# Kernel tuning notes

Hardware: AMD Instinct MI355X
Metric: run time of the kernel (lower is better)

## Reference

```python
import jax, jax.numpy as jnp
import numpy as np


def setup_inputs() -> dict:
    key = jax.random.key(0)
    k1, k2, k3 = jax.random.split(key, 3)
    B, D, C = 16384, 1024, 14
    z_image = jax.random.normal(k1, (B, D), dtype=jnp.float32)
    z_text = jax.random.normal(k2, (B, D), dtype=jnp.float32)
    labels = jax.random.randint(k3, (B, C), 0, 2, dtype=jnp.int32)
    return {"z_image": z_image, "z_text": z_text, "labels": labels}


def _margins(labels):
    # labels: [B, C] binary; imposter index j = (i+1) % B -> roll by -1
    lj = jnp.roll(labels, -1, axis=0)
    equal = jnp.all(labels == lj, axis=1)                     # [B]
    n = jnp.sum(labels | lj, axis=1).astype(jnp.float32)      # union size
    d = jnp.sum(labels ^ lj, axis=1).astype(jnp.float32)      # hamming diff
    m = jnp.where(n > 0, jnp.maximum(0.5, d / jnp.maximum(n, 1.0)), 0.5)
    return jnp.where(equal, 0.0, m)                           # [B]


def reference(z_image, z_text, labels):
    # similarity_function == 'dot' (default path of the torch module)
    margin = _margins(labels)                                  # [B]
    paired = jnp.sum(z_image * z_text, axis=1)                 # dot(img_i, txt_i)
    imp_img = jnp.sum(jnp.roll(z_image, -1, axis=0) * z_text, axis=1)  # dot(img_j, txt_i)
    imp_txt = jnp.sum(jnp.roll(z_text, -1, axis=0) * z_image, axis=1)  # dot(txt_j, img_i)
    loss_img = jnp.mean(jax.nn.relu(imp_img - paired + margin))
    loss_txt = jnp.mean(jax.nn.relu(imp_txt - paired + margin))
    return loss_img + loss_txt
```

## Files before the change

kernel.cpp:

```cpp
#include <hip/hip_runtime.h>


constexpr int D      = 1024;
constexpr int C      = 14;
constexpr int TPR    = 16;
constexpr int RPB    = 256 / TPR;
constexpr int CHUNKS = D / 4 / TPR;

__device__ __forceinline__ float dot4(const float4 x, const float4 y) {
    return x.x * y.x + x.y * y.y + x.z * y.z + x.w * y.w;
}

__global__ __launch_bounds__(256, 2) void rank_phase1(
    const float* __restrict__ zi, const float* __restrict__ zt,
    const int* __restrict__ labels, float* __restrict__ partial, int B)
{
    const int t    = threadIdx.x;
    const int rsub = t >> 4;
    const int csub = t & 15;
    const int row  = blockIdx.x * RPB + rsub;
    const int M    = B - 1;
    const int nrow = (row + 1) & M;

    float margin = 0.f;
    if (csub == 0) {
        const int2* La = (const int2*)(labels + (size_t)row  * C);
        const int2* Lb = (const int2*)(labels + (size_t)nrow * C);
        int dv = 0, nv = 0;
        #pragma unroll
        for (int q = 0; q < C / 2; ++q) {
            const int2 x = La[q];
            const int2 y = Lb[q];
            dv += (x.x ^ y.x) + (x.y ^ y.y);
            nv += (x.x | y.x) + (x.y | y.y);
        }
        margin = (dv == 0) ? 0.f : fmaxf(0.5f, (float)dv / (float)nv);
    }

    const float4* Ar  = (const float4*)(zi + (size_t)row  * D);
    const float4* Br  = (const float4*)(zt + (size_t)row  * D);
    const float4* Ar1 = (const float4*)(zi + (size_t)nrow * D);
    const float4* Br1 = (const float4*)(zt + (size_t)nrow * D);

    float p = 0.f, ii = 0.f, it = 0.f;
    #pragma unroll
    for (int c = 0; c < CHUNKS; ++c) {
        const int idx = csub + TPR * c;
        const float4 a  = Ar [idx];
        const float4 b  = Br [idx];
        const float4 a1 = Ar1[idx];
        const float4 b1 = Br1[idx];
        p  += dot4(a,  b);
        ii += dot4(a1, b);
        it += dot4(b1, a);
    }

    #pragma unroll
    for (int off = 1; off < TPR; off <<= 1) {
        p  += __shfl_xor(p,  off, 64);
        ii += __shfl_xor(ii, off, 64);
        it += __shfl_xor(it, off, 64);
    }

    __shared__ float sm[RPB];
    if (csub == 0)
        sm[rsub] = fmaxf(ii - p + margin, 0.f)
                 + fmaxf(it - p + margin, 0.f);
    __syncthreads();
    if (t == 0) {
        float s = 0.f;
        #pragma unroll
        for (int k = 0; k < RPB; ++k) s += sm[k];
        partial[blockIdx.x] = s;
    }
}

__global__ __launch_bounds__(256) void rank_phase2(
    const float* __restrict__ partial, float* __restrict__ out,
    int npart, float invB)
{
    float s = 0.f;
    for (int i = threadIdx.x; i < npart; i += 256) s += partial[i];
    #pragma unroll
    for (int off = 32; off > 0; off >>= 1) s += __shfl_down(s, off, 64);
    __shared__ float sm[4];
    if ((threadIdx.x & 63) == 0) sm[threadIdx.x >> 6] = s;
    __syncthreads();
    if (threadIdx.x == 0)
        out[0] = (sm[0] + sm[1] + sm[2] + sm[3]) * invB;
}

extern "C" void kernel_launch(void* const* d_in, const int* in_sizes, int n_in,
                              void* d_out, int out_size, void* d_ws, size_t ws_size,
                              hipStream_t stream) {
    const float* zi     = (const float*)d_in[0];
    const float* zt     = (const float*)d_in[1];
    const int*   labels = (const int*)d_in[2];
    float*       out    = (float*)d_out;
    float*       ws     = (float*)d_ws;

    const int B      = in_sizes[0] / D;
    const int blocks = B / RPB;

    rank_phase1<<<blocks, 256, 0, stream>>>(zi, zt, labels, ws, B);
    rank_phase2<<<1, 256, 0, stream>>>(ws, out, blocks, 1.0f / (float)B);
}
```

Measured before the change: 155.7 us.

## Share neighbor rows via wave shuffles and split columns across waves

Each wave now processes eight consecutive rows over a quarter of the columns and obtains the next row's vectors through lane shuffles instead of reloading them from memory, with only a single halo row loaded extra. Loads use nontemporal hints to avoid polluting cache. Margin computation and the per-row hinge are moved to a final per-block step after combining wave partials in shared memory. This reduces redundant global reads but adds shuffle work and a divergent halo load.

```diff
diff --git a/kernel.cpp b/kernel.cpp
--- a/kernel.cpp
+++ b/kernel.cpp
@@ -1,31 +1,96 @@
 #include <hip/hip_runtime.h>
 
 
-constexpr int D      = 1024;
-constexpr int C      = 14;
-constexpr int TPR    = 16;
-constexpr int RPB    = 256 / TPR;
-constexpr int CHUNKS = D / 4 / TPR;
+constexpr int D   = 1024;
+constexpr int C   = 14;
+constexpr int RPB = 8;
+constexpr int CPR = D / 4;
 
-__device__ __forceinline__ float dot4(const float4 x, const float4 y) {
+typedef float f4 __attribute__((ext_vector_type(4)));
+
+__device__ __forceinline__ float dot4(const f4 x, const f4 y) {
     return x.x * y.x + x.y * y.y + x.z * y.z + x.w * y.w;
 }
 
-__global__ __launch_bounds__(256, 2) void rank_phase1(
+__device__ __forceinline__ f4 shfl_down4(const f4 v) {
+    f4 r;
+    r.x = __shfl_down(v.x, 8, 64);
+    r.y = __shfl_down(v.y, 8, 64);
+    r.z = __shfl_down(v.z, 8, 64);
+    r.w = __shfl_down(v.w, 8, 64);
+    return r;
+}
+
+__global__ __launch_bounds__(256) void rank_phase1(
     const float* __restrict__ zi, const float* __restrict__ zt,
     const int* __restrict__ labels, float* __restrict__ partial, int B)
 {
-    const int t    = threadIdx.x;
-    const int rsub = t >> 4;
-    const int csub = t & 15;
-    const int row  = blockIdx.x * RPB + rsub;
+    const int wave = threadIdx.x >> 6;
+    const int lane = threadIdx.x & 63;
+    const int r0   = blockIdx.x * RPB;
     const int M    = B - 1;
-    const int nrow = (row + 1) & M;
 
-    float margin = 0.f;
-    if (csub == 0) {
-        const int2* La = (const int2*)(labels + (size_t)row  * C);
-        const int2* Lb = (const int2*)(labels + (size_t)nrow * C);
+    const int row_off = lane >> 3;
+    const int cl      = lane & 7;
+    const int row     = r0 + row_off;
+    const int hrow    = (r0 + RPB) & M;
+
+    const f4* ZI = (const f4*)zi;
+    const f4* ZT = (const f4*)zt;
+
+    const int cb = wave * (CPR / 4);
+
+    float p = 0.f, ii = 0.f, it = 0.f;
+
+    #pragma unroll
+    for (int i = 0; i < CPR / 4 / 8; ++i) {
+        const int c = cb + 8 * i + cl;
+        const f4 a = __builtin_nontemporal_load(&ZI[(size_t)row * CPR + c]);
+        const f4 b = __builtin_nontemporal_load(&ZT[(size_t)row * CPR + c]);
+
+        f4 ha, hb;
+        if (row_off == 7) {
+            ha = __builtin_nontemporal_load(&ZI[(size_t)hrow * CPR + c]);
+            hb = __builtin_nontemporal_load(&ZT[(size_t)hrow * CPR + c]);
+        }
+
+        f4 aN = shfl_down4(a);
+        f4 bN = shfl_down4(b);
+        if (row_off == 7) { aN = ha; bN = hb; }
+
+        p  += dot4(a,  b);
+        ii += dot4(aN, b);
+        it += dot4(bN, a);
+    }
+
+    #pragma unroll
+    for (int off = 1; off < 8; off <<= 1) {
+        p  += __shfl_xor(p,  off, 64);
+        ii += __shfl_xor(ii, off, 64);
+        it += __shfl_xor(it, off, 64);
+    }
+
+    __shared__ float sm[4][RPB][3];
+    if (cl == 0) {
+        sm[wave][row_off][0] = p;
+        sm[wave][row_off][1] = ii;
+        sm[wave][row_off][2] = it;
+    }
+    __syncthreads();
+
+    if (threadIdx.x < RPB) {
+        const int k = threadIdx.x;
+        float ps = 0.f, is = 0.f, ts = 0.f;
+        #pragma unroll
+        for (int w = 0; w < 4; ++w) {
+            ps += sm[w][k][0];
+            is += sm[w][k][1];
+            ts += sm[w][k][2];
+        }
+        const int ra = r0 + k;
+        const int rb = (ra + 1) & M;
+        const int2* La = (const int2*)(labels + (size_t)ra * C);
+        const int2* Lb = (const int2*)(labels + (size_t)rb * C);
         int dv = 0, nv = 0;
         #pragma unroll
         for (int q = 0; q < C / 2; ++q) {
@@ -34,44 +99,13 @@
             dv += (x.x ^ y.x) + (x.y ^ y.y);
             nv += (x.x | y.x) + (x.y | y.y);
         }
-        margin = (dv == 0) ? 0.f : fmaxf(0.5f, (float)dv / (float)nv);
-    }
-
-    const float4* Ar  = (const float4*)(zi + (size_t)row  * D);
-    const float4* Br  = (const float4*)(zt + (size_t)row  * D);
-    const float4* Ar1 = (const float4*)(zi + (size_t)nrow * D);
-    const float4* Br1 = (const float4*)(zt + (size_t)nrow * D);
-
-    float p = 0.f, ii = 0.f, it = 0.f;
-    #pragma unroll
-    for (int c = 0; c < CHUNKS; ++c) {
-        const int idx = csub + TPR * c;
-        const float4 a  = Ar [idx];
-        const float4 b  = Br [idx];
-        const float4 a1 = Ar1[idx];
-        const float4 b1 = Br1[idx];
-        p  += dot4(a,  b);
-        ii += dot4(a1, b);
-        it += dot4(b1, a);
-    }
-
-    #pragma unroll
-    for (int off = 1; off < TPR; off <<= 1) {
-        p  += __shfl_xor(p,  off, 64);
-        ii += __shfl_xor(ii, off, 64);
-        it += __shfl_xor(it, off, 64);
-    }
-
-    __shared__ float sm[RPB];
-    if (csub == 0)
-        sm[rsub] = fmaxf(ii - p + margin, 0.f)
-                 + fmaxf(it - p + margin, 0.f);
-    __syncthreads();
-    if (t == 0) {
-        float s = 0.f;
+        const float m = (dv == 0) ? 0.f
+                                  : fmaxf(0.5f, (float)dv / (float)nv);
+        float v = fmaxf(is - ps + m, 0.f) + fmaxf(ts - ps + m, 0.f);
         #pragma unroll
-        for (int k = 0; k < RPB; ++k) s += sm[k];
-        partial[blockIdx.x] = s;
+        for (int off = 1; off < RPB; off <<= 1)
+            v += __shfl_xor(v, off, 64);
+        if (k == 0) partial[blockIdx.x] = v;
     }
 }
 
```

New measurement: 150.8 us. 1.03x faster.
